# Kernel tuning notes

Hardware: AMD Instinct MI355X
Metric: run time of the kernel (lower is better)

## Reference

```python
import jax, jax.numpy as jnp
from jax import lax
import numpy as np

B, T, H, OUT = 8, 1500, 1280, 4096
MAXTOK = 375
N_INNER = 3  # 1 mandatory integrate-and-fire iteration + 2 gated extras (alpha<1 => 1 suffices)


def _forward_cif(hidden, alphas, num_tokens, max_tok):
    # hidden: [B, T, D], alphas: [B, T], num_tokens: [B] int32
    Bv, Tv, _ = hidden.shape
    nm1 = num_tokens - 1
    bidx = jnp.arange(Bv)

    def step(carry, xs):
        integrate, token_index = carry  # [B] float, [B] int32
        alpha_t, not_last = xs
        col = jnp.zeros((Bv, max_tok), alphas.dtype)
        alpha = alpha_t
        alpha_needed = 1.0 - integrate
        integrate = integrate + alpha
        ready = integrate >= 1.0
        remainds = jnp.zeros_like(alpha)
        active = jnp.any(ready) | True  # first body iteration always runs (do-while)
        active = jnp.asarray(True)
        for _ in range(N_INNER):
            n_int = jnp.where(ready, integrate - 1.0, integrate)
            a_int = jnp.where(ready, alpha_needed, alpha)
            n_col = col.at[bidx, token_index].set(a_int)
            n_rem = alpha - a_int
            n_tok = jnp.minimum(token_index + ready.astype(token_index.dtype), nm1)
            n_ready = n_int >= 1.0
            integrate = jnp.where(active, n_int, integrate)
            col = jnp.where(active, n_col, col)
            remainds = jnp.where(active, n_rem, remainds)
            token_index = jnp.where(active, n_tok, token_index)
            alpha = jnp.where(active, n_rem, alpha)
            alpha_needed = jnp.where(active, jnp.ones_like(alpha_needed), alpha_needed)
            ready = jnp.where(active, n_ready, jnp.zeros_like(ready))
            active = active & jnp.any(ready)
        # torch adds remainds into column t at step t+1 (so last column never gets it)
        col = jnp.where(not_last, col.at[bidx, token_index].add(remainds), col)
        return (integrate, token_index), col

    init = (jnp.zeros((Bv,), alphas.dtype), jnp.zeros((Bv,), jnp.int32))
    xs = (alphas.T, jnp.arange(Tv) < Tv - 1)  # per-step alpha column, not-last flag
    _, cols = lax.scan(step, init, xs)  # cols: [T, B, max_tok]
    weights = jnp.transpose(cols, (1, 2, 0))  # [B, max_tok, T]
    return jnp.einsum('bmt,btd->bmd', weights, hidden)


def setup_inputs() -> dict:
    key = jax.random.key(0)
    ks = jax.random.split(key, 4)
    audio_features = jax.random.normal(ks[0], (B, T, H), jnp.float32)
    num_tokens = jax.random.randint(ks[1], (B,), 100, MAXTOK + 1).astype(jnp.int32)
    rms_w = jnp.ones((H,), jnp.float32) * 0.4
    cif_w = jax.random.normal(ks[2], (H - 1, H), jnp.float32) / np.sqrt(H - 1)
    cif_b = jnp.zeros((H,), jnp.float32)
    text_w = jax.random.normal(ks[3], (H, OUT), jnp.float32) / np.sqrt(H)
    text_b = jnp.zeros((OUT,), jnp.float32)
    return dict(audio_features=audio_features, num_tokens=num_tokens, rms_w=rms_w,
                cif_w=cif_w, cif_b=cif_b, text_w=text_w, text_b=text_b, max_tokens=MAXTOK)


def reference(audio_features, num_tokens, rms_w, cif_w, cif_b, text_w, text_b, max_tokens):
    alphas = jax.nn.sigmoid(audio_features[:, :, -1])  # [B, T]
    pred_num_tokens = alphas.sum(-1)  # [B]
    alphas = alphas * (num_tokens.astype(alphas.dtype) / pred_num_tokens)[:, None]
    h = _forward_cif(audio_features[:, :, :-1], alphas, num_tokens, max_tokens)  # [B, M, H-1]
    h = h @ cif_w + cif_b  # cif_proj -> [B, M, H]
    d = h.shape[-1]
    rms = jnp.sqrt(jnp.sum(h * h, axis=-1, keepdims=True) / d + 1e-6)
    h = h / rms * rms_w  # RMSNorm(post_ln)
    h = h @ text_w + text_b  # text_proj -> [B, M, OUT]
    return h, pred_num_tokens
```

## Files before the change

### kernel.cpp

```cpp
#include <hip/hip_runtime.h>
#include <hip/hip_bf16.h>
#include <stdint.h>

#define B_ 8
#define T_ 1500
#define TPAD 1504
#define H_ 1280
#define HM1 1279
#define OUT_ 4096
#define MTOK 375
#define MROWS (B_*MTOK)
#define KPAD 1280

typedef __attribute__((ext_vector_type(8))) short bf16x8;
typedef __attribute__((ext_vector_type(4))) float f32x4;
typedef unsigned short u16;

static __device__ __forceinline__ u16 f2bf(float f) {
    unsigned int x = __float_as_uint(f);
    unsigned int r = (x + 0x7fffu + ((x >> 16) & 1u)) >> 16;
    return (u16)r;
}
static __device__ __forceinline__ void glds16(const u16* g, u16* l) {
    __builtin_amdgcn_global_load_lds(
        (const __attribute__((address_space(1))) void*)g,
        (__attribute__((address_space(3))) void*)l, 16, 0, 0);
}

__global__ __launch_bounds__(256) void k_front(
    const float* __restrict__ audio, const int* __restrict__ num_tokens,
    const float* __restrict__ rms_w,
    float* __restrict__ pred_out,
    int* __restrict__ tok0, float* __restrict__ w0a,
    int* __restrict__ tok1, float* __restrict__ w1a,
    int* __restrict__ lo, int* __restrict__ hi,
    float* __restrict__ h_sumsq,
    const float* __restrict__ cif_w, const float* __restrict__ text_w,
    u16* __restrict__ cwt, u16* __restrict__ twt)
{
    __shared__ float smem[3524];
    const int tid = threadIdx.x;

    if (blockIdx.x < B_) {
        const int b = blockIdx.x;
        float* al = smem;
        float* ip = smem + TPAD;
        float* red = smem + 2*TPAD;
        int*   redI = (int*)(smem + 2*TPAD + 256);
        float* scale_sh = smem + 2*TPAD + 512;

        float sig[6];
        float s = 0.f;
        #pragma unroll
        for (int i = 0; i < 6; ++i) {
            int t = tid + i*256;
            sig[i] = 0.f;
            if (t < T_) {
                float x = audio[((size_t)b*T_ + t)*H_ + (H_-1)];
                sig[i] = 1.f / (1.f + expf(-x));
                s += sig[i];
            }
        }
        red[tid] = s; __syncthreads();
        for (int off = 128; off > 0; off >>= 1) {
            if (tid < off) red[tid] += red[tid+off];
            __syncthreads();
        }
        if (tid == 0) {
            float pred = red[0];
            pred_out[b] = pred;
            *scale_sh = (float)num_tokens[b] / pred;
        }
        __syncthreads();
        float scale = *scale_sh;
        #pragma unroll
        for (int i = 0; i < 6; ++i) {
            int t = tid + i*256;
            if (t < T_) al[t] = sig[i] * scale;
        }
        if (tid < TPAD - T_) al[T_ + tid] = 0.f;
        for (int m = tid; m < MTOK; m += 256) {
            lo[b*MTOK+m] = T_; hi[b*MTOK+m] = 0;
            h_sumsq[b*MTOK+m] = 0.f;
        }
        if (tid == 0) lo[b*MTOK] = 0;
        __syncthreads();

        if (tid == 0) {
            float integ = 0.f;
            float4 c0 = *(const float4*)&al[0];
            float4 c1 = *(const float4*)&al[4];
            float4 c2 = *(const float4*)&al[8];
            float4 c3 = *(const float4*)&al[12];
            for (int t = 0; t < TPAD; t += 16) {
                float4 n0, n1, n2, n3;
                if (t + 16 < TPAD) {
                    n0 = *(const float4*)&al[t+16];
                    n1 = *(const float4*)&al[t+20];
                    n2 = *(const float4*)&al[t+24];
                    n3 = *(const float4*)&al[t+28];
                }
                float4 o0, o1, o2, o3;
                float sx;
                o0.x = integ; sx = integ + c0.x; integ = sx - floorf(sx);
                o0.y = integ; sx = integ + c0.y; integ = sx - floorf(sx);
                o0.z = integ; sx = integ + c0.z; integ = sx - floorf(sx);
                o0.w = integ; sx = integ + c0.w; integ = sx - floorf(sx);
                o1.x = integ; sx = integ + c1.x; integ = sx - floorf(sx);
                o1.y = integ; sx = integ + c1.y; integ = sx - floorf(sx);
                o1.z = integ; sx = integ + c1.z; integ = sx - floorf(sx);
                o1.w = integ; sx = integ + c1.w; integ = sx - floorf(sx);
                o2.x = integ; sx = integ + c2.x; integ = sx - floorf(sx);
                o2.y = integ; sx = integ + c2.y; integ = sx - floorf(sx);
                o2.z = integ; sx = integ + c2.z; integ = sx - floorf(sx);
                o2.w = integ; sx = integ + c2.w; integ = sx - floorf(sx);
                o3.x = integ; sx = integ + c3.x; integ = sx - floorf(sx);
                o3.y = integ; sx = integ + c3.y; integ = sx - floorf(sx);
                o3.z = integ; sx = integ + c3.z; integ = sx - floorf(sx);
                o3.w = integ; sx = integ + c3.w; integ = sx - floorf(sx);
                *(float4*)&ip[t+0]  = o0;
                *(float4*)&ip[t+4]  = o1;
                *(float4*)&ip[t+8]  = o2;
                *(float4*)&ip[t+12] = o3;
                c0 = n0; c1 = n1; c2 = n2; c3 = n3;
            }
        }
        __syncthreads();

        const int t0 = tid * 6;
        const int nm1 = num_tokens[b] - 1;
        int fires[6];
        int cnt = 0;
        if (t0 < T_) {
            #pragma unroll
            for (int j = 0; j < 6; ++j) {
                int t = t0 + j;
                float sx = ip[t] + al[t];
                fires[j] = (sx >= 1.f) ? 1 : 0;
                cnt += fires[j];
            }
        }
        redI[tid] = cnt; __syncthreads();
        #pragma unroll
        for (int off = 1; off < 256; off <<= 1) {
            int v = redI[tid];
            if (tid >= off) v += redI[tid - off];
            __syncthreads();
            redI[tid] = v;
            __syncthreads();
        }
        if (t0 < T_) {
            int F = redI[tid] - cnt;
            const int base = b*T_;
            #pragma unroll
            for (int j = 0; j < 6; ++j) {
                int t = t0 + j;
                float a = al[t], ipv = ip[t];
                int fire = fires[j];
                F += fire;
                int tk1 = min(F, nm1);
                int tk0 = min(F - fire, nm1);
                float w0 = fire ? (1.f - ipv) : a;
                float w1 = (t < T_-1) ? (a - w0) : 0.f;
                tok0[base+t] = tk0;  w0a[base+t] = w0;
                tok1[base+t] = tk1;  w1a[base+t] = w1;
                if (tk1 != tk0) {
                    hi[b*MTOK + tk0] = t + 1;
                    lo[b*MTOK + tk1] = t;
                }
                if (t == T_-1) hi[b*MTOK + tk1] = T_;
            }
        }
    } else {
        float (*tile)[33] = (float(*)[33])smem;
        int blk = blockIdx.x - B_;
        const float* src; u16* dst; int R, C, bx, by; bool scaled;
        if (blk < 1600) { src = cif_w;  dst = cwt; R = HM1; C = H_;   bx = blk % 40;  by = blk / 40;  scaled = false; }
        else { blk -= 1600; src = text_w; dst = twt; R = H_;  C = OUT_; bx = blk % 128; by = blk / 128; scaled = true; }
        int c0 = bx * 32, r0 = by * 32;
        int lx = tid & 31, ly = tid >> 5;
        #pragma unroll
        for (int j = 0; j < 4; ++j) {
            int r = r0 + ly + j*8;
            tile[ly + j*8][lx] = (r < R) ? src[(size_t)r*C + c0 + lx] : 0.f;
        }
        __syncthreads();
        float rw = scaled ? rms_w[r0 + lx] : 1.f;
        #pragma unroll
        for (int j = 0; j < 4; ++j) {
            int c = c0 + ly + j*8;
            dst[(size_t)c*KPAD + r0 + lx] = f2bf(tile[lx][ly + j*8] * rw);
        }
    }
}

__global__ __launch_bounds__(256) void k3_pool(
    const float* __restrict__ audio,
    const int* __restrict__ tok0, const float* __restrict__ w0a,
    const int* __restrict__ tok1, const float* __restrict__ w1a,
    const int* __restrict__ lo, const int* __restrict__ hi,
    u16* __restrict__ h1b)
{
    __shared__ float wl[1536];
    const int bm = blockIdx.x;
    const int b = bm / MTOK, m = bm % MTOK;
    const int l = lo[bm], h = hi[bm];
    const int tid = threadIdx.x;
    const int len = h - l;

    for (int j = tid; j < len; j += 256) {
        int i0 = b*T_ + l + j;
        float w = 0.f;
        if (tok0[i0] == m) w += w0a[i0];
        if (tok1[i0] == m) w += w1a[i0];
        wl[j] = w;
    }
    __syncthreads();

    const int d4 = tid * 4;
    const int d1 = 1024 + tid;
    const float* rowp = audio + (size_t)(b*T_ + l) * H_;
    float4 acc4 = make_float4(0.f, 0.f, 0.f, 0.f);
    float acc1 = 0.f;
    #pragma unroll 4
    for (int j = 0; j < len; ++j) {
        float w = wl[j];
        const float* row = rowp + (size_t)j * H_;
        float4 r4 = *(const float4*)(row + d4);
        float r1 = (d1 < HM1) ? row[d1] : 0.f;
        acc4.x += w * r4.x; acc4.y += w * r4.y;
        acc4.z += w * r4.z; acc4.w += w * r4.w;
        acc1 += w * r1;
    }
    u16* dst = h1b + (size_t)bm * KPAD;
    ushort4 o;
    o.x = f2bf(acc4.x); o.y = f2bf(acc4.y); o.z = f2bf(acc4.z); o.w = f2bf(acc4.w);
    *(ushort4*)&dst[d4] = o;
    dst[d1] = (d1 < HM1) ? f2bf(acc1) : (u16)0;
}

#define WAITVM(N) asm volatile("s_waitcnt vmcnt(" #N ")" ::: "memory")

template<int TM, bool CIF>
__global__ __launch_bounds__(256, 3) void mfma_gemm_bt(
    const u16* __restrict__ A, const u16* __restrict__ Bt,
    const float* __restrict__ bias, void* __restrict__ Cv,
    float* __restrict__ h_sumsq, int M, int N)
{
    constexpr int K = KPAD;
    constexpr int NT = K / 32;
    constexpr int RA = TM / 64;
    constexpr int MI = 4;
    constexpr int NI = (TM == 128) ? 4 : 2;
    __shared__ u16 sA[3][TM*32];
    __shared__ u16 sB[3][128*32];
    const int tid = threadIdx.x;
    const int m0 = blockIdx.y * TM, n0 = blockIdx.x * 128;
    const int wave = tid >> 6, lane = tid & 63;
    const int wm = (TM == 128) ? (wave & 1) * 64 : 0;
    const int wn = (TM == 128) ? (wave >> 1) * 64 : wave * 32;
    const int lrow = lane & 15, quad = lane >> 4;

    const int r0 = tid >> 2, sl = tid & 3;
    const int q0 = sl ^ (r0 & 3) ^ ((r0 >> 2) & 3);
    const u16* Ag[RA];
    #pragma unroll
    for (int p = 0; p < RA; ++p)
        Ag[p] = A + (size_t)min(m0 + r0 + 64*p, M - 1) * K + q0 * 8;
    const u16* Bg[2];
    #pragma unroll
    for (int p = 0; p < 2; ++p)
        Bg[p] = Bt + (size_t)(n0 + r0 + 64*p) * K + q0 * 8;

    int offA[MI], offB[NI];
    #pragma unroll
    for (int i = 0; i < MI; ++i) {
        int m = wm + i*16 + lrow;
        offA[i] = m*32 + (quad ^ (m & 3) ^ ((m >> 2) & 3)) * 8;
    }
    #pragma unroll
    for (int i = 0; i < NI; ++i) {
        int n = wn + i*16 + lrow;
        offB[i] = n*32 + (quad ^ (n & 3) ^ ((n >> 2) & 3)) * 8;
    }

    u16 *Ac = sA[0], *An = sA[1], *Af = sA[2];
    u16 *Bc = sB[0], *Bn = sB[1], *Bf = sB[2];

    auto stage = [&](int kk, u16* da, u16* db) {
        #pragma unroll
        for (int p = 0; p < RA; ++p) glds16(Ag[p] + kk, da + (tid + 256*p)*8);
        #pragma unroll
        for (int p = 0; p < 2;  ++p) glds16(Bg[p] + kk, db + (tid + 256*p)*8);
    };

    f32x4 acc[MI][NI] = {};

    stage(0,  Ac, Bc);
    stage(32, An, Bn);

    for (int t = 0; t < NT - 1; ++t) {
        if constexpr (TM == 128) WAITVM(4); else WAITVM(3);
        __builtin_amdgcn_s_barrier();
        asm volatile("" ::: "memory");
        if (t + 2 < NT) stage((t + 2) * 32, Af, Bf);
        bf16x8 af[MI], bfr[NI];
        #pragma unroll
        for (int i = 0; i < MI; ++i) af[i]  = *(const bf16x8*)&Ac[offA[i]];
        #pragma unroll
        for (int i = 0; i < NI; ++i) bfr[i] = *(const bf16x8*)&Bc[offB[i]];
        __builtin_amdgcn_s_setprio(1);
        #pragma unroll
        for (int mi = 0; mi < MI; ++mi)
            #pragma unroll
            for (int ni = 0; ni < NI; ++ni)
                acc[mi][ni] = __builtin_amdgcn_mfma_f32_16x16x32_bf16(
                    af[mi], bfr[ni], acc[mi][ni], 0, 0, 0);
        __builtin_amdgcn_s_setprio(0);
        u16* ta = Ac; Ac = An; An = Af; Af = ta;
        u16* tb = Bc; Bc = Bn; Bn = Bf; Bf = tb;
    }
    {
        WAITVM(0);
        __builtin_amdgcn_s_barrier();
        asm volatile("" ::: "memory");
        bf16x8 af[MI], bfr[NI];
        #pragma unroll
        for (int i = 0; i < MI; ++i) af[i]  = *(const bf16x8*)&Ac[offA[i]];
        #pragma unroll
        for (int i = 0; i < NI; ++i) bfr[i] = *(const bf16x8*)&Bc[offB[i]];
        __builtin_amdgcn_s_setprio(1);
        #pragma unroll
        for (int mi = 0; mi < MI; ++mi)
            #pragma unroll
            for (int ni = 0; ni < NI; ++ni)
                acc[mi][ni] = __builtin_amdgcn_mfma_f32_16x16x32_bf16(
                    af[mi], bfr[ni], acc[mi][ni], 0, 0, 0);
        __builtin_amdgcn_s_setprio(0);
    }

    float bv[NI];
    #pragma unroll
    for (int ni = 0; ni < NI; ++ni) bv[ni] = bias[n0 + wn + ni*16 + lrow];

    #pragma unroll
    for (int mi = 0; mi < MI; ++mi) {
        #pragma unroll
        for (int r = 0; r < 4; ++r) {
            int row = m0 + wm + mi*16 + quad*4 + r;
            if (CIF) {
                float ss = 0.f;
                #pragma unroll
                for (int ni = 0; ni < NI; ++ni) {
                    float v = acc[mi][ni][r] + bv[ni];
                    ss += v * v;
                    if (row < M)
                        ((u16*)Cv)[(size_t)row*N + (n0 + wn + ni*16 + lrow)] = f2bf(v);
                }
                ss += __shfl_xor(ss, 1);
                ss += __shfl_xor(ss, 2);
                ss += __shfl_xor(ss, 4);
                ss += __shfl_xor(ss, 8);
                if (lrow == 0 && row < M) atomicAdd(&h_sumsq[row], ss);
            } else {
                float inv = 1.f;
                if (row < M)
                    inv = 1.f / sqrtf(h_sumsq[row] / (float)H_ + 1e-6f);
                #pragma unroll
                for (int ni = 0; ni < NI; ++ni) {
                    if (row < M)
                        ((float*)Cv)[(size_t)row*N + (n0 + wn + ni*16 + lrow)] =
                            acc[mi][ni][r] * inv + bv[ni];
                }
            }
        }
    }
}

extern "C" void kernel_launch(void* const* d_in, const int* in_sizes, int n_in,
                              void* d_out, int out_size, void* d_ws, size_t ws_size,
                              hipStream_t stream) {
    (void)in_sizes; (void)n_in; (void)out_size; (void)ws_size;
    const float* audio      = (const float*)d_in[0];
    const int*   num_tokens = (const int*)d_in[1];
    const float* rms_w      = (const float*)d_in[2];
    const float* cif_w      = (const float*)d_in[3];
    const float* cif_b      = (const float*)d_in[4];
    const float* text_w     = (const float*)d_in[5];
    const float* text_b     = (const float*)d_in[6];

    float* out  = (float*)d_out;
    float* pred = out + (size_t)MROWS * OUT_;

    char* ws = (char*)d_ws;
    float* h_sumsq = (float*)(ws + 0);
    float* w0a  = (float*)(ws + 48000);
    float* w1a  = (float*)(ws + 96000);
    int*   tok0 = (int*)  (ws + 144000);
    int*   tok1 = (int*)  (ws + 192000);
    int*   lo   = (int*)  (ws + 240000);
    int*   hi   = (int*)  (ws + 252000);
    u16* h1b = (u16*)(ws + 264192);
    u16* cwt = (u16*)(ws + 7944192);
    u16* twt = (u16*)(ws + 11220992);
    u16* hX  = (u16*)(ws + 21706752);

    k_front<<<B_ + 1600 + 5120, 256, 0, stream>>>(
        audio, num_tokens, rms_w, pred, tok0, w0a, tok1, w1a, lo, hi,
        h_sumsq, cif_w, text_w, cwt, twt);
    k3_pool<<<MROWS, 256, 0, stream>>>(audio, tok0, w0a, tok1, w1a, lo, hi, h1b);
    mfma_gemm_bt<64, true><<<dim3(H_/128, (MROWS+63)/64), 256, 0, stream>>>(
        h1b, cwt, cif_b, hX, h_sumsq, MROWS, H_);
    mfma_gemm_bt<128, false><<<dim3(OUT_/128, (MROWS+127)/128), 256, 0, stream>>>(
        hX, twt, text_b, out, h_sumsq, MROWS, OUT_);
}
```

Measured before the change: 237.5 us.

## Replace both GEMMs with a 256x256-tile, 512-thread double-buffered MFMA kernel

Both projection GEMMs now use one kernel with 256x256 output tiles, 8 waves per block and K-steps of 64 in a two-buffer LDS ring. Each wave computes a 128x64 sub-tile, which raises register-level reuse of A and B fragments and cuts global traffic per FLOP. In exchange the grids shrink sharply: the first GEMM gets 60 blocks and the second 192, on a GPU with 256 CUs. The LDS footprint is about 128 KB per block, so only one block can be resident per CU. Prefetch wait handling in the loop now depends on __syncthreads rather than an explicit vmcnt, which may serialize loads against compute.

```diff
diff --git a/kernel.cpp b/kernel.cpp
--- a/kernel.cpp
+++ b/kernel.cpp
@@ -15,6 +15,7 @@
 typedef __attribute__((ext_vector_type(8))) short bf16x8;
 typedef __attribute__((ext_vector_type(4))) float f32x4;
 typedef unsigned short u16;
+typedef unsigned int u32;
 
 static __device__ __forceinline__ u16 f2bf(float f) {
     unsigned int x = __float_as_uint(f);
@@ -239,123 +240,106 @@
     dst[d1] = (d1 < HM1) ? f2bf(acc1) : (u16)0;
 }
 
-#define WAITVM(N) asm volatile("s_waitcnt vmcnt(" #N ")" ::: "memory")
-
-template<int TM, bool CIF>
-__global__ __launch_bounds__(256, 3) void mfma_gemm_bt(
+template<bool CIF>
+__global__ __launch_bounds__(512, 2) void gemm256(
     const u16* __restrict__ A, const u16* __restrict__ Bt,
     const float* __restrict__ bias, void* __restrict__ Cv,
     float* __restrict__ h_sumsq, int M, int N)
 {
     constexpr int K = KPAD;
-    constexpr int NT = K / 32;
-    constexpr int RA = TM / 64;
-    constexpr int MI = 4;
-    constexpr int NI = (TM == 128) ? 4 : 2;
-    __shared__ u16 sA[3][TM*32];
-    __shared__ u16 sB[3][128*32];
+    constexpr int NT = K / 64;
+    __shared__ u16 sA[2][256*64];
+    __shared__ u16 sB[2][256*64];
     const int tid = threadIdx.x;
-    const int m0 = blockIdx.y * TM, n0 = blockIdx.x * 128;
     const int wave = tid >> 6, lane = tid & 63;
-    const int wm = (TM == 128) ? (wave & 1) * 64 : 0;
-    const int wn = (TM == 128) ? (wave >> 1) * 64 : wave * 32;
+    const int wr = wave >> 2, wc = wave & 3;
     const int lrow = lane & 15, quad = lane >> 4;
-
-    const int r0 = tid >> 2, sl = tid & 3;
-    const int q0 = sl ^ (r0 & 3) ^ ((r0 >> 2) & 3);
-    const u16* Ag[RA];
-    #pragma unroll
-    for (int p = 0; p < RA; ++p)
-        Ag[p] = A + (size_t)min(m0 + r0 + 64*p, M - 1) * K + q0 * 8;
-    const u16* Bg[2];
-    #pragma unroll
-    for (int p = 0; p < 2; ++p)
-        Bg[p] = Bt + (size_t)(n0 + r0 + 64*p) * K + q0 * 8;
-
-    int offA[MI], offB[NI];
-    #pragma unroll
-    for (int i = 0; i < MI; ++i) {
-        int m = wm + i*16 + lrow;
-        offA[i] = m*32 + (quad ^ (m & 3) ^ ((m >> 2) & 3)) * 8;
-    }
-    #pragma unroll
-    for (int i = 0; i < NI; ++i) {
-        int n = wn + i*16 + lrow;
-        offB[i] = n*32 + (quad ^ (n & 3) ^ ((n >> 2) & 3)) * 8;
-    }
-
-    u16 *Ac = sA[0], *An = sA[1], *Af = sA[2];
-    u16 *Bc = sB[0], *Bn = sB[1], *Bf = sB[2];
-
-    auto stage = [&](int kk, u16* da, u16* db) {
-        #pragma unroll
-        for (int p = 0; p < RA; ++p) glds16(Ag[p] + kk, da + (tid + 256*p)*8);
-        #pragma unroll
-        for (int p = 0; p < 2;  ++p) glds16(Bg[p] + kk, db + (tid + 256*p)*8);
-    };
-
-    f32x4 acc[MI][NI] = {};
-
-    stage(0,  Ac, Bc);
-    stage(32, An, Bn);
-
-    for (int t = 0; t < NT - 1; ++t) {
-        if constexpr (TM == 128) WAITVM(4); else WAITVM(3);
-        __builtin_amdgcn_s_barrier();
-        asm volatile("" ::: "memory");
-        if (t + 2 < NT) stage((t + 2) * 32, Af, Bf);
-        bf16x8 af[MI], bfr[NI];
-        #pragma unroll
-        for (int i = 0; i < MI; ++i) af[i]  = *(const bf16x8*)&Ac[offA[i]];
-        #pragma unroll
-        for (int i = 0; i < NI; ++i) bfr[i] = *(const bf16x8*)&Bc[offB[i]];
-        __builtin_amdgcn_s_setprio(1);
-        #pragma unroll
-        for (int mi = 0; mi < MI; ++mi)
-            #pragma unroll
-            for (int ni = 0; ni < NI; ++ni)
-                acc[mi][ni] = __builtin_amdgcn_mfma_f32_16x16x32_bf16(
-                    af[mi], bfr[ni], acc[mi][ni], 0, 0, 0);
-        __builtin_amdgcn_s_setprio(0);
-        u16* ta = Ac; Ac = An; An = Af; Af = ta;
-        u16* tb = Bc; Bc = Bn; Bn = Bf; Bf = tb;
-    }
-    {
-        WAITVM(0);
-        __builtin_amdgcn_s_barrier();
-        asm volatile("" ::: "memory");
-        bf16x8 af[MI], bfr[NI];
-        #pragma unroll
-        for (int i = 0; i < MI; ++i) af[i]  = *(const bf16x8*)&Ac[offA[i]];
-        #pragma unroll
-        for (int i = 0; i < NI; ++i) bfr[i] = *(const bf16x8*)&Bc[offB[i]];
-        __builtin_amdgcn_s_setprio(1);
-        #pragma unroll
-        for (int mi = 0; mi < MI; ++mi)
-            #pragma unroll
-            for (int ni = 0; ni < NI; ++ni)
-                acc[mi][ni] = __builtin_amdgcn_mfma_f32_16x16x32_bf16(
-                    af[mi], bfr[ni], acc[mi][ni], 0, 0, 0);
-        __builtin_amdgcn_s_setprio(0);
-    }
-
-    float bv[NI];
-    #pragma unroll
-    for (int ni = 0; ni < NI; ++ni) bv[ni] = bias[n0 + wn + ni*16 + lrow];
-
-    #pragma unroll
-    for (int mi = 0; mi < MI; ++mi) {
-        #pragma unroll
-        for (int r = 0; r < 4; ++r) {
-            int row = m0 + wm + mi*16 + quad*4 + r;
+    const int m0 = blockIdx.y * 256, n0 = blockIdx.x * 256;
+
+    const int rS = tid >> 3;
+    const int cS = (tid & 7) ^ (rS & 7);
+    u32 aoff[4], boff[4];
+    #pragma unroll
+    for (int p = 0; p < 4; ++p) {
+        aoff[p] = (u32)(min(m0 + rS + 64*p, M - 1) * K + cS*8);
+        boff[p] = (u32)((n0 + rS + 64*p) * K + cS*8);
+    }
+
+    const int csw = (quad ^ (lrow & 7)) << 3;
+    int offA[8], offB[4];
+    #pragma unroll
+    for (int mi = 0; mi < 8; ++mi)
+        offA[mi] = (wr*128 + mi*16 + lrow)*64 + csw;
+    #pragma unroll
+    for (int ni = 0; ni < 4; ++ni)
+        offB[ni] = (wc*64 + ni*16 + lrow)*64 + csw;
+
+    f32x4 acc[8][4] = {};
+
+    #pragma unroll
+    for (int p = 0; p < 4; ++p) {
+        glds16(A + aoff[p],      (u16*)sA[0] + (tid + 512*p)*8);
+        glds16(Bt + boff[p],     (u16*)sB[0] + (tid + 512*p)*8);
+    }
+    #pragma unroll
+    for (int p = 0; p < 4; ++p) {
+        glds16(A + aoff[p] + 64, (u16*)sA[1] + (tid + 512*p)*8);
+        glds16(Bt + boff[p] + 64,(u16*)sB[1] + (tid + 512*p)*8);
+    }
+    asm volatile("s_waitcnt vmcnt(8)" ::: "memory");
+    __builtin_amdgcn_s_barrier();
+
+    for (int t = 0; t < NT; ++t) {
+        const u16* bufA = sA[t & 1];
+        const u16* bufB = sB[t & 1];
+        #pragma unroll
+        for (int ks = 0; ks < 2; ++ks) {
+            const int kx = ks ? 32 : 0;
+            bf16x8 bfr[4], afr[8];
+            #pragma unroll
+            for (int ni = 0; ni < 4; ++ni)
+                bfr[ni] = *(const bf16x8*)&bufB[offB[ni] ^ kx];
+            #pragma unroll
+            for (int mi = 0; mi < 8; ++mi)
+                afr[mi] = *(const bf16x8*)&bufA[offA[mi] ^ kx];
+            #pragma unroll
+            for (int mi = 0; mi < 8; ++mi)
+                #pragma unroll
+                for (int ni = 0; ni < 4; ++ni)
+                    acc[mi][ni] = __builtin_amdgcn_mfma_f32_16x16x32_bf16(
+                        afr[mi], bfr[ni], acc[mi][ni], 0, 0, 0);
+        }
+        __syncthreads();
+        if (t + 2 < NT) {
+            const u32 k0 = (u32)(t + 2) * 64;
+            u16* dA = (u16*)sA[t & 1];
+            u16* dB = (u16*)sB[t & 1];
+            #pragma unroll
+            for (int p = 0; p < 4; ++p) {
+                glds16(A + aoff[p] + k0,  dA + (tid + 512*p)*8);
+                glds16(Bt + boff[p] + k0, dB + (tid + 512*p)*8);
+            }
+        }
+    }
+
+    float bv[4];
+    #pragma unroll
+    for (int ni = 0; ni < 4; ++ni)
+        bv[ni] = bias[n0 + wc*64 + ni*16 + lrow];
+
+    #pragma unroll
+    for (int mi = 0; mi < 8; ++mi) {
+        #pragma unroll
+        for (int rr = 0; rr < 4; ++rr) {
+            int row = m0 + wr*128 + mi*16 + quad*4 + rr;
             if (CIF) {
                 float ss = 0.f;
                 #pragma unroll
-                for (int ni = 0; ni < NI; ++ni) {
-                    float v = acc[mi][ni][r] + bv[ni];
+                for (int ni = 0; ni < 4; ++ni) {
+                    float v = acc[mi][ni][rr] + bv[ni];
                     ss += v * v;
                     if (row < M)
-                        ((u16*)Cv)[(size_t)row*N + (n0 + wn + ni*16 + lrow)] = f2bf(v);
+                        ((u16*)Cv)[(size_t)row*N + (n0 + wc*64 + ni*16 + lrow)] = f2bf(v);
                 }
                 ss += __shfl_xor(ss, 1);
                 ss += __shfl_xor(ss, 2);
@@ -367,10 +351,10 @@
                 if (row < M)
                     inv = 1.f / sqrtf(h_sumsq[row] / (float)H_ + 1e-6f);
                 #pragma unroll
-                for (int ni = 0; ni < NI; ++ni) {
+                for (int ni = 0; ni < 4; ++ni) {
                     if (row < M)
-                        ((float*)Cv)[(size_t)row*N + (n0 + wn + ni*16 + lrow)] =
-                            acc[mi][ni][r] * inv + bv[ni];
+                        ((float*)Cv)[(size_t)row*N + (n0 + wc*64 + ni*16 + lrow)] =
+                            acc[mi][ni][rr] * inv + bv[ni];
                 }
             }
         }
@@ -409,8 +393,8 @@
         audio, num_tokens, rms_w, pred, tok0, w0a, tok1, w1a, lo, hi,
         h_sumsq, cif_w, text_w, cwt, twt);
     k3_pool<<<MROWS, 256, 0, stream>>>(audio, tok0, w0a, tok1, w1a, lo, hi, h1b);
-    mfma_gemm_bt<64, true><<<dim3(H_/128, (MROWS+63)/64), 256, 0, stream>>>(
+    gemm256<true><<<dim3(H_/256, (MROWS+255)/256), 512, 0, stream>>>(
         h1b, cwt, cif_b, hX, h_sumsq, MROWS, H_);
-    mfma_gemm_bt<128, false><<<dim3(OUT_/128, (MROWS+127)/128), 256, 0, stream>>>(
+    gemm256<false><<<dim3(OUT_/256, (MROWS+255)/256), 512, 0, stream>>>(
         hX, twt, text_b, out, h_sumsq, MROWS, OUT_);
 }
```

After: 264.6 us. 1.11x slower.

## Replace triple-buffered LDS pipeline with double buffering and syncthreads

Applied to the files above, without the earlier changes.

Rewrites the GEMM main loop to use two LDS buffers instead of three, unrolled by two, issuing the next tile's global-to-LDS loads before computing on the current tile and separating stages with __syncthreads. It drops the explicit vmcnt waits, the raw s_barrier and the s_setprio hints. This halves the prefetch distance and lowers LDS use, which may allow higher occupancy. The cost is that the full barrier waits on all outstanding loads each step, so load latency is less hidden.

```diff
diff --git a/kernel.cpp b/kernel.cpp
--- a/kernel.cpp
+++ b/kernel.cpp
@@ -239,8 +239,6 @@
     dst[d1] = (d1 < HM1) ? f2bf(acc1) : (u16)0;
 }
 
-#define WAITVM(N) asm volatile("s_waitcnt vmcnt(" #N ")" ::: "memory")
-
 template<int TM, bool CIF>
 __global__ __launch_bounds__(256, 3) void mfma_gemm_bt(
     const u16* __restrict__ A, const u16* __restrict__ Bt,
@@ -252,8 +250,8 @@
     constexpr int RA = TM / 64;
     constexpr int MI = 4;
     constexpr int NI = (TM == 128) ? 4 : 2;
-    __shared__ u16 sA[3][TM*32];
-    __shared__ u16 sB[3][128*32];
+    __shared__ u16 sA[2][TM*32];
+    __shared__ u16 sB[2][128*32];
     const int tid = threadIdx.x;
     const int m0 = blockIdx.y * TM, n0 = blockIdx.x * 128;
     const int wave = tid >> 6, lane = tid & 63;
@@ -284,59 +282,55 @@
         offB[i] = n*32 + (quad ^ (n & 3) ^ ((n >> 2) & 3)) * 8;
     }
 
-    u16 *Ac = sA[0], *An = sA[1], *Af = sA[2];
-    u16 *Bc = sB[0], *Bn = sB[1], *Bf = sB[2];
-
-    auto stage = [&](int kk, u16* da, u16* db) {
-        #pragma unroll
-        for (int p = 0; p < RA; ++p) glds16(Ag[p] + kk, da + (tid + 256*p)*8);
-        #pragma unroll
-        for (int p = 0; p < 2;  ++p) glds16(Bg[p] + kk, db + (tid + 256*p)*8);
-    };
-
     f32x4 acc[MI][NI] = {};
 
-    stage(0,  Ac, Bc);
-    stage(32, An, Bn);
-
-    for (int t = 0; t < NT - 1; ++t) {
-        if constexpr (TM == 128) WAITVM(4); else WAITVM(3);
-        __builtin_amdgcn_s_barrier();
-        asm volatile("" ::: "memory");
-        if (t + 2 < NT) stage((t + 2) * 32, Af, Bf);
-        bf16x8 af[MI], bfr[NI];
-        #pragma unroll
-        for (int i = 0; i < MI; ++i) af[i]  = *(const bf16x8*)&Ac[offA[i]];
-        #pragma unroll
-        for (int i = 0; i < NI; ++i) bfr[i] = *(const bf16x8*)&Bc[offB[i]];
-        __builtin_amdgcn_s_setprio(1);
-        #pragma unroll
-        for (int mi = 0; mi < MI; ++mi)
-            #pragma unroll
-            for (int ni = 0; ni < NI; ++ni)
-                acc[mi][ni] = __builtin_amdgcn_mfma_f32_16x16x32_bf16(
-                    af[mi], bfr[ni], acc[mi][ni], 0, 0, 0);
-        __builtin_amdgcn_s_setprio(0);
-        u16* ta = Ac; Ac = An; An = Af; Af = ta;
-        u16* tb = Bc; Bc = Bn; Bn = Bf; Bf = tb;
-    }
-    {
-        WAITVM(0);
-        __builtin_amdgcn_s_barrier();
-        asm volatile("" ::: "memory");
-        bf16x8 af[MI], bfr[NI];
-        #pragma unroll
-        for (int i = 0; i < MI; ++i) af[i]  = *(const bf16x8*)&Ac[offA[i]];
-        #pragma unroll
-        for (int i = 0; i < NI; ++i) bfr[i] = *(const bf16x8*)&Bc[offB[i]];
-        __builtin_amdgcn_s_setprio(1);
-        #pragma unroll
-        for (int mi = 0; mi < MI; ++mi)
-            #pragma unroll
-            for (int ni = 0; ni < NI; ++ni)
-                acc[mi][ni] = __builtin_amdgcn_mfma_f32_16x16x32_bf16(
-                    af[mi], bfr[ni], acc[mi][ni], 0, 0, 0);
-        __builtin_amdgcn_s_setprio(0);
+    #pragma unroll
+    for (int p = 0; p < RA; ++p) glds16(Ag[p], &sA[0][(tid + 256*p)*8]);
+    #pragma unroll
+    for (int p = 0; p < 2;  ++p) glds16(Bg[p], &sB[0][(tid + 256*p)*8]);
+    __syncthreads();
+
+    for (int t = 0; t < NT; t += 2) {
+        {
+            const int k1 = (t + 1) * 32;
+            #pragma unroll
+            for (int p = 0; p < RA; ++p) glds16(Ag[p] + k1, &sA[1][(tid + 256*p)*8]);
+            #pragma unroll
+            for (int p = 0; p < 2;  ++p) glds16(Bg[p] + k1, &sB[1][(tid + 256*p)*8]);
+            bf16x8 af[MI], bfr[NI];
+            #pragma unroll
+            for (int i = 0; i < MI; ++i) af[i]  = *(const bf16x8*)&sA[0][offA[i]];
+            #pragma unroll
+            for (int i = 0; i < NI; ++i) bfr[i] = *(const bf16x8*)&sB[0][offB[i]];
+            #pragma unroll
+            for (int mi = 0; mi < MI; ++mi)
+                #pragma unroll
+                for (int ni = 0; ni < NI; ++ni)
+                    acc[mi][ni] = __builtin_amdgcn_mfma_f32_16x16x32_bf16(
+                        af[mi], bfr[ni], acc[mi][ni], 0, 0, 0);
+            __syncthreads();
+        }
+        {
+            const int k2 = (t + 2) * 32;
+            if (t + 2 < NT) {
+                #pragma unroll
+                for (int p = 0; p < RA; ++p) glds16(Ag[p] + k2, &sA[0][(tid + 256*p)*8]);
+                #pragma unroll
+                for (int p = 0; p < 2;  ++p) glds16(Bg[p] + k2, &sB[0][(tid + 256*p)*8]);
+            }
+            bf16x8 af[MI], bfr[NI];
+            #pragma unroll
+            for (int i = 0; i < MI; ++i) af[i]  = *(const bf16x8*)&sA[1][offA[i]];
+            #pragma unroll
+            for (int i = 0; i < NI; ++i) bfr[i] = *(const bf16x8*)&sB[1][offB[i]];
+            #pragma unroll
+            for (int mi = 0; mi < MI; ++mi)
+                #pragma unroll
+                for (int ni = 0; ni < NI; ++ni)
+                    acc[mi][ni] = __builtin_amdgcn_mfma_f32_16x16x32_bf16(
+                        af[mi], bfr[ni], acc[mi][ni], 0, 0, 0);
+            __syncthreads();
+        }
     }
 
     float bv[NI];
```

After: 239.0 us. No clear change (+0.6%).
